# Performance work log

Measured on AMD Instinct MI355X. Metric: run time of the kernel, lower is better.

The kernel has to match this reference:

```python
import jax, jax.numpy as jnp
import numpy as np

N = 8192
D_IN = 512
D_HID = 256
D_OUT = 128
NEG_SLOPE = 0.25
MASK_VAL = -1.0e12
EDGE_PROB = 0.004  # avg degree ~33


def _leaky(x):
    return jax.nn.leaky_relu(x, NEG_SLOPE)


def setup_inputs() -> dict:
    key = jax.random.key(0)
    ks = jax.random.split(key, 9)
    x = jax.random.normal(ks[0], (N, D_IN), jnp.float32)
    # sparse-ish normalized adjacency, stored dense (torch uses sparse mm / to_dense)
    vals = jax.random.uniform(ks[1], (N, N), jnp.float32)
    mask = jax.random.uniform(ks[2], (N, N)) < EDGE_PROB
    adj = jnp.where(mask, vals, 0.0).astype(jnp.float32)
    W1 = jax.random.normal(ks[3], (D_IN, D_HID), jnp.float32) * (2.0 / (D_IN + D_HID)) ** 0.5
    b1 = jnp.zeros((D_HID,), jnp.float32)
    W2 = jax.random.normal(ks[4], (D_HID, D_HID), jnp.float32) * (1.0 / D_HID) ** 0.5
    b2 = jnp.zeros((D_HID,), jnp.float32)
    Wg = jax.random.normal(ks[5], (D_HID, D_OUT), jnp.float32) * (2.0 / (D_HID + D_OUT)) ** 0.5
    a = jax.random.normal(ks[6], (2 * D_OUT, 1), jnp.float32) * 0.1
    return dict(x=x, adj=adj, W1=W1, b1=b1, W2=W2, b2=b2, Wg=Wg, a=a)


def reference(x, adj, W1, b1, W2, b2, Wg, a):
    # GCN layer 1: adj @ (x @ W1) + b1, leaky_relu (dropout p=0 / eval -> identity)
    x1 = _leaky(adj @ (x @ W1) + b1)
    # GCN layer 2
    x2 = _leaky(adj @ (x1 @ W2) + b2)
    # GAT layer: h = x2 @ Wg; e[i,j] = leaky_relu([h_i || h_j] @ a)
    # identical to leaky_relu((h@a1)_i + (h@a2)_j) without the O(N^2*2F) concat
    h = x2 @ Wg                              # [N, D_OUT]
    a1 = a[:D_OUT, 0]
    a2 = a[D_OUT:, 0]
    e = _leaky((h @ a1)[:, None] + (h @ a2)[None, :])  # [N, N]
    att = jnp.where(adj > 0, e, MASK_VAL)
    att = jax.nn.softmax(att, axis=1)
    h_prime = att @ h                        # [N, D_OUT] (concat=False -> no elu)
    out = _leaky(h_prime)
    mu = out[:, : D_OUT // 2]
    logvar = out[:, D_OUT // 2 :]
    return mu, logvar
```

## Files before the change

kernel.cpp:

```cpp
#include <hip/hip_runtime.h>

typedef unsigned short u16;
typedef __bf16 bf16x8 __attribute__((ext_vector_type(8)));
typedef float f32x4 __attribute__((ext_vector_type(4)));

#define NROW 8192
#define CAP 128
#define D_IN 512
#define D_HID 256
#define D_OUT 128

__device__ __forceinline__ float leaky_f(float x) { return x > 0.f ? x : 0.25f * x; }

__device__ __forceinline__ u16 f2bf_rne(float f) {
  unsigned u = __float_as_uint(f);
  u += 0x7fffu + ((u >> 16) & 1u);
  return (u16)(u >> 16);
}
__device__ __forceinline__ void split_bf16(float f, u16& hi, u16& lo) {
  hi = f2bf_rne(f);
  float fh = __uint_as_float(((unsigned)hi) << 16);
  lo = f2bf_rne(f - fh);
}

__global__ __launch_bounds__(256) void k_csr(const float* __restrict__ adj,
    int* __restrict__ cnt, int* __restrict__ cols, float* __restrict__ vals) {
  int i = blockIdx.x;
  __shared__ int c;
  if (threadIdx.x == 0) c = 0;
  __syncthreads();
  const float4* row = (const float4*)(adj + (size_t)i * NROW);
  for (int j4 = threadIdx.x; j4 < NROW / 4; j4 += 256) {
    float4 v = row[j4];
    int base = j4 * 4;
    if (v.x > 0.f) { int s = atomicAdd(&c, 1); if (s < CAP) { cols[i*CAP+s] = base;   vals[i*CAP+s] = v.x; } }
    if (v.y > 0.f) { int s = atomicAdd(&c, 1); if (s < CAP) { cols[i*CAP+s] = base+1; vals[i*CAP+s] = v.y; } }
    if (v.z > 0.f) { int s = atomicAdd(&c, 1); if (s < CAP) { cols[i*CAP+s] = base+2; vals[i*CAP+s] = v.z; } }
    if (v.w > 0.f) { int s = atomicAdd(&c, 1); if (s < CAP) { cols[i*CAP+s] = base+3; vals[i*CAP+s] = v.w; } }
  }
  __syncthreads();
  if (threadIdx.x == 0) cnt[i] = (c < CAP) ? c : CAP;
}

__global__ __launch_bounds__(256) void k_pack_x(const float* __restrict__ X, u16* __restrict__ Ap) {
  size_t id = (size_t)blockIdx.x * 256 + threadIdx.x;
  int k = (int)(id & 511);
  size_t i = id >> 9;
  float f = X[id];
  u16 hi, lo; split_bf16(f, hi, lo);
  size_t ro = i * 1536;
  Ap[ro + k] = hi; Ap[ro + 512 + k] = hi; Ap[ro + 1024 + k] = lo;
}

__global__ __launch_bounds__(256) void k_pack_w(const float* __restrict__ W, u16* __restrict__ Bt,
                                                int K, int Nc) {
  int id = blockIdx.x * 256 + threadIdx.x;
  if (id >= K * Nc) return;
  int n = id % Nc, k = id / Nc;
  float f = W[id];
  u16 hi, lo; split_bf16(f, hi, lo);
  size_t ro = (size_t)n * 3 * K;
  Bt[ro + k] = hi; Bt[ro + K + k] = lo; Bt[ro + 2*K + k] = hi;
}

__global__ __launch_bounds__(256) void k_gemm(const u16* __restrict__ A, const u16* __restrict__ Bt,
    float* __restrict__ C, int N, int K) {
  __shared__ u16 As[64][40];
  __shared__ u16 Bs[64][40];
  int tid = threadIdx.x;
  int bm = blockIdx.y * 64, bn = blockIdx.x * 64;
  int wave = tid >> 6, lane = tid & 63, l15 = lane & 15, quad = lane >> 4;
  f32x4 acc[4] = {};
  int r = tid >> 2, kc = (tid & 3) << 3;
  for (int k0 = 0; k0 < K; k0 += 32) {
    uint4 av = *(const uint4*)(A + (size_t)(bm + r) * K + k0 + kc);
    uint4 bv = *(const uint4*)(Bt + (size_t)(bn + r) * K + k0 + kc);
    *(uint4*)(&As[r][kc]) = av;
    *(uint4*)(&Bs[r][kc]) = bv;
    __syncthreads();
    bf16x8 af = *(const bf16x8*)(&As[wave * 16 + l15][quad * 8]);
#pragma unroll
    for (int c2 = 0; c2 < 4; ++c2) {
      bf16x8 bfr = *(const bf16x8*)(&Bs[c2 * 16 + l15][quad * 8]);
      acc[c2] = __builtin_amdgcn_mfma_f32_16x16x32_bf16(af, bfr, acc[c2], 0, 0, 0);
    }
    __syncthreads();
  }
#pragma unroll
  for (int c2 = 0; c2 < 4; ++c2)
#pragma unroll
    for (int rg = 0; rg < 4; ++rg) {
      int rowi = bm + wave * 16 + quad * 4 + rg;
      int coli = bn + c2 * 16 + l15;
      C[(size_t)rowi * N + coli] = acc[c2][rg];
    }
}

__global__ __launch_bounds__(256) void k_spmm_pack(const float* __restrict__ Hin,
    const float* __restrict__ bias, const int* __restrict__ cnt,
    const int* __restrict__ cols, const float* __restrict__ vals, u16* __restrict__ Ap) {
  int i = blockIdx.x, t = threadIdx.x;
  __shared__ int sc[CAP];
  __shared__ float sv[CAP];
  int n = cnt[i];
  if (t < n) { sc[t] = cols[i * CAP + t]; sv[t] = vals[i * CAP + t]; }
  __syncthreads();
  float acc = bias[t];
  for (int k = 0; k < n; ++k)
    acc = fmaf(sv[k], Hin[(size_t)sc[k] * D_HID + t], acc);
  acc = leaky_f(acc);
  u16 hi, lo; split_bf16(acc, hi, lo);
  size_t ro = (size_t)i * 768;
  Ap[ro + t] = hi; Ap[ro + 256 + t] = hi; Ap[ro + 512 + t] = lo;
}

__global__ __launch_bounds__(64) void k_sdot(const float* __restrict__ h,
    const float* __restrict__ a, float* __restrict__ s1, float* __restrict__ s2) {
  int i = blockIdx.x, t = threadIdx.x;
  float v0 = h[(size_t)i * D_OUT + t], v1 = h[(size_t)i * D_OUT + 64 + t];
  float p1 = v0 * a[t] + v1 * a[64 + t];
  float p2 = v0 * a[128 + t] + v1 * a[192 + t];
  for (int o = 32; o > 0; o >>= 1) { p1 += __shfl_down(p1, o); p2 += __shfl_down(p2, o); }
  if (t == 0) { s1[i] = p1; s2[i] = p2; }
}

__global__ __launch_bounds__(128) void k_attn(const float* __restrict__ h,
    const float* __restrict__ s1, const float* __restrict__ s2,
    const int* __restrict__ cnt, const int* __restrict__ cols, float* __restrict__ out) {
  int i = blockIdx.x, t = threadIdx.x;
  __shared__ int sc[CAP];
  __shared__ float sw[CAP];
  __shared__ float sred[2];
  int n = cnt[i];
  float s1i = s1[i];
  if (t < n) { int c = cols[i * CAP + t]; sc[t] = c; sw[t] = leaky_f(s1i + s2[c]); }
  __syncthreads();
  if (t < 64) {
    float m = -1e30f;
    if (t < n) m = sw[t];
    if (t + 64 < n) m = fmaxf(m, sw[t + 64]);
    for (int o = 32; o > 0; o >>= 1) m = fmaxf(m, __shfl_down(m, o));
    if (t == 0) sred[0] = m;
  }
  __syncthreads();
  float mx = sred[0];
  if (t < n) sw[t] = expf(sw[t] - mx);
  __syncthreads();
  if (t < 64) {
    float s = 0.f;
    if (t < n) s = sw[t];
    if (t + 64 < n) s += sw[t + 64];
    for (int o = 32; o > 0; o >>= 1) s += __shfl_down(s, o);
    if (t == 0) sred[1] = s;
  }
  __syncthreads();
  float inv = (n > 0) ? 1.0f / sred[1] : 0.f;
  float acc = 0.f;
  for (int k = 0; k < n; ++k)
    acc = fmaf(sw[k], h[(size_t)sc[k] * D_OUT + t], acc);
  acc = leaky_f(acc * inv);
  if (t < 64) out[(size_t)i * 64 + t] = acc;
  else        out[(size_t)NROW * 64 + (size_t)i * 64 + (t - 64)] = acc;
}

extern "C" void kernel_launch(void* const* d_in, const int* in_sizes, int n_in,
                              void* d_out, int out_size, void* d_ws, size_t ws_size,
                              hipStream_t stream) {
  const float* x   = (const float*)d_in[0];
  const float* adj = (const float*)d_in[1];
  const float* W1  = (const float*)d_in[2];
  const float* b1  = (const float*)d_in[3];
  const float* W2  = (const float*)d_in[4];
  const float* b2  = (const float*)d_in[5];
  const float* Wg  = (const float*)d_in[6];
  const float* a   = (const float*)d_in[7];
  float* out = (float*)d_out;

  char* ws = (char*)d_ws;
  int*   row_cnt  = (int*)  (ws + 0);
  int*   row_cols = (int*)  (ws + 32768);
  float* row_vals = (float*)(ws + 4227072);
  u16*   B1t      = (u16*)  (ws + 8421376);
  u16*   B2t      = (u16*)  (ws + 9207808);
  u16*   B3t      = (u16*)  (ws + 9601024);
  float* s1       = (float*)(ws + 9797632);
  float* s2       = (float*)(ws + 9830400);
  float* h        = (float*)(ws + 9863168);
  float* H0T2     = (float*)(ws + 14057472);
  u16*   Apack    = (u16*)  (ws + 22446080);

  k_csr<<<NROW, 256, 0, stream>>>(adj, row_cnt, row_cols, row_vals);
  k_pack_x<<<(NROW * D_IN) / 256, 256, 0, stream>>>(x, Apack);
  k_pack_w<<<(D_IN * D_HID + 255) / 256, 256, 0, stream>>>(W1, B1t, D_IN, D_HID);
  k_pack_w<<<(D_HID * D_HID + 255) / 256, 256, 0, stream>>>(W2, B2t, D_HID, D_HID);
  k_pack_w<<<(D_HID * D_OUT + 255) / 256, 256, 0, stream>>>(Wg, B3t, D_HID, D_OUT);
  k_gemm<<<dim3(D_HID / 64, NROW / 64), 256, 0, stream>>>(Apack, B1t, H0T2, D_HID, 3 * D_IN);
  k_spmm_pack<<<NROW, 256, 0, stream>>>(H0T2, b1, row_cnt, row_cols, row_vals, Apack);
  k_gemm<<<dim3(D_HID / 64, NROW / 64), 256, 0, stream>>>(Apack, B2t, H0T2, D_HID, 3 * D_HID);
  k_spmm_pack<<<NROW, 256, 0, stream>>>(H0T2, b2, row_cnt, row_cols, row_vals, Apack);
  k_gemm<<<dim3(D_OUT / 64, NROW / 64), 256, 0, stream>>>(Apack, B3t, h, D_OUT, 3 * D_HID);
  k_sdot<<<NROW, 64, 0, stream>>>(h, a, s1, s2);
  k_attn<<<NROW, 128, 0, stream>>>(h, s1, s2, row_cnt, row_cols, out);
}
```

Baseline: 527.5 us.

## Enlarge GEMM tiles to 128x64 with K-step 64 and merge pack kernels

The split-bf16 GEMM now computes a 128x64 output tile per block, with each wave holding a 2x4 grid of MFMA accumulators. The K step grows from 32 to 64 and the LDS rows are padded to 72 elements, so each synchronisation covers more MFMA work and each B fragment is reused across two A fragments. The four packing kernels are merged into one launch that branches on block index. The tradeoff is higher register use, which may lower occupancy, and half as many blocks in the grid.

Result: no change. 517.9 us (-1.8%).

```diff
diff --git a/kernel.cpp b/kernel.cpp
--- a/kernel.cpp
+++ b/kernel.cpp
@@ -42,19 +42,25 @@
   if (threadIdx.x == 0) cnt[i] = (c < CAP) ? c : CAP;
 }
 
-__global__ __launch_bounds__(256) void k_pack_x(const float* __restrict__ X, u16* __restrict__ Ap) {
-  size_t id = (size_t)blockIdx.x * 256 + threadIdx.x;
-  int k = (int)(id & 511);
-  size_t i = id >> 9;
-  float f = X[id];
-  u16 hi, lo; split_bf16(f, hi, lo);
-  size_t ro = i * 1536;
-  Ap[ro + k] = hi; Ap[ro + 512 + k] = hi; Ap[ro + 1024 + k] = lo;
-}
-
-__global__ __launch_bounds__(256) void k_pack_w(const float* __restrict__ W, u16* __restrict__ Bt,
-                                                int K, int Nc) {
-  int id = blockIdx.x * 256 + threadIdx.x;
+__global__ __launch_bounds__(256) void k_pack_all(const float* __restrict__ X, u16* __restrict__ Ap,
+    const float* __restrict__ W1, u16* __restrict__ B1,
+    const float* __restrict__ W2, u16* __restrict__ B2,
+    const float* __restrict__ Wg, u16* __restrict__ B3) {
+  int b = blockIdx.x;
+  if (b < 16384) {
+    size_t id = (size_t)b * 256 + threadIdx.x;
+    int k = (int)(id & 511);
+    size_t i = id >> 9;
+    float f = X[id];
+    u16 hi, lo; split_bf16(f, hi, lo);
+    size_t ro = i * 1536;
+    Ap[ro + k] = hi; Ap[ro + 512 + k] = hi; Ap[ro + 1024 + k] = lo;
+    return;
+  }
+  const float* W; u16* Bt; int K, Nc, id;
+  if (b < 16896)      { W = W1; Bt = B1; K = D_IN;  Nc = D_HID; id = (b - 16384) * 256 + threadIdx.x; }
+  else if (b < 17152) { W = W2; Bt = B2; K = D_HID; Nc = D_HID; id = (b - 16896) * 256 + threadIdx.x; }
+  else                { W = Wg; Bt = B3; K = D_HID; Nc = D_OUT; id = (b - 17152) * 256 + threadIdx.x; }
   if (id >= K * Nc) return;
   int n = id % Nc, k = id / Nc;
   float f = W[id];
@@ -65,35 +71,51 @@
 
 __global__ __launch_bounds__(256) void k_gemm(const u16* __restrict__ A, const u16* __restrict__ Bt,
     float* __restrict__ C, int N, int K) {
-  __shared__ u16 As[64][40];
-  __shared__ u16 Bs[64][40];
+  __shared__ u16 As[128 * 72];
+  __shared__ u16 Bs[64 * 72];
   int tid = threadIdx.x;
-  int bm = blockIdx.y * 64, bn = blockIdx.x * 64;
+  int bm = blockIdx.y * 128, bn = blockIdx.x * 64;
   int wave = tid >> 6, lane = tid & 63, l15 = lane & 15, quad = lane >> 4;
-  f32x4 acc[4] = {};
-  int r = tid >> 2, kc = (tid & 3) << 3;
-  for (int k0 = 0; k0 < K; k0 += 32) {
-    uint4 av = *(const uint4*)(A + (size_t)(bm + r) * K + k0 + kc);
-    uint4 bv = *(const uint4*)(Bt + (size_t)(bn + r) * K + k0 + kc);
-    *(uint4*)(&As[r][kc]) = av;
-    *(uint4*)(&Bs[r][kc]) = bv;
+  f32x4 acc[2][4] = {};
+  int ar = tid >> 1, ac = (tid & 1) * 32;
+  int br = tid >> 2, bc = (tid & 3) * 16;
+  const u16* Arow = A + (size_t)(bm + ar) * K + ac;
+  const u16* Brow = Bt + (size_t)(bn + br) * K + bc;
+  for (int k0 = 0; k0 < K; k0 += 64) {
+#pragma unroll
+    for (int j = 0; j < 4; ++j)
+      *(uint4*)(&As[ar * 72 + ac + j * 8]) = *(const uint4*)(Arow + k0 + j * 8);
+#pragma unroll
+    for (int j = 0; j < 2; ++j)
+      *(uint4*)(&Bs[br * 72 + bc + j * 8]) = *(const uint4*)(Brow + k0 + j * 8);
     __syncthreads();
-    bf16x8 af = *(const bf16x8*)(&As[wave * 16 + l15][quad * 8]);
-#pragma unroll
-    for (int c2 = 0; c2 < 4; ++c2) {
-      bf16x8 bfr = *(const bf16x8*)(&Bs[c2 * 16 + l15][quad * 8]);
-      acc[c2] = __builtin_amdgcn_mfma_f32_16x16x32_bf16(af, bfr, acc[c2], 0, 0, 0);
+#pragma unroll
+    for (int kk = 0; kk < 64; kk += 32) {
+      bf16x8 af[2], bf[4];
+#pragma unroll
+      for (int r = 0; r < 2; ++r)
+        af[r] = *(const bf16x8*)(&As[(wave * 32 + r * 16 + l15) * 72 + kk + quad * 8]);
+#pragma unroll
+      for (int c = 0; c < 4; ++c)
+        bf[c] = *(const bf16x8*)(&Bs[(c * 16 + l15) * 72 + kk + quad * 8]);
+#pragma unroll
+      for (int r = 0; r < 2; ++r)
+#pragma unroll
+        for (int c = 0; c < 4; ++c)
+          acc[r][c] = __builtin_amdgcn_mfma_f32_16x16x32_bf16(af[r], bf[c], acc[r][c], 0, 0, 0);
     }
     __syncthreads();
   }
 #pragma unroll
-  for (int c2 = 0; c2 < 4; ++c2)
-#pragma unroll
-    for (int rg = 0; rg < 4; ++rg) {
-      int rowi = bm + wave * 16 + quad * 4 + rg;
-      int coli = bn + c2 * 16 + l15;
-      C[(size_t)rowi * N + coli] = acc[c2][rg];
-    }
+  for (int r = 0; r < 2; ++r)
+#pragma unroll
+    for (int c = 0; c < 4; ++c)
+#pragma unroll
+      for (int rg = 0; rg < 4; ++rg) {
+        int rowi = bm + wave * 32 + r * 16 + quad * 4 + rg;
+        int coli = bn + c * 16 + l15;
+        C[(size_t)rowi * N + coli] = acc[r][c][rg];
+      }
 }
 
 __global__ __launch_bounds__(256) void k_spmm_pack(const float* __restrict__ Hin,
@@ -190,15 +212,12 @@
   u16*   Apack    = (u16*)  (ws + 22446080);
 
   k_csr<<<NROW, 256, 0, stream>>>(adj, row_cnt, row_cols, row_vals);
-  k_pack_x<<<(NROW * D_IN) / 256, 256, 0, stream>>>(x, Apack);
-  k_pack_w<<<(D_IN * D_HID + 255) / 256, 256, 0, stream>>>(W1, B1t, D_IN, D_HID);
-  k_pack_w<<<(D_HID * D_HID + 255) / 256, 256, 0, stream>>>(W2, B2t, D_HID, D_HID);
-  k_pack_w<<<(D_HID * D_OUT + 255) / 256, 256, 0, stream>>>(Wg, B3t, D_HID, D_OUT);
-  k_gemm<<<dim3(D_HID / 64, NROW / 64), 256, 0, stream>>>(Apack, B1t, H0T2, D_HID, 3 * D_IN);
+  k_pack_all<<<17280, 256, 0, stream>>>(x, Apack, W1, B1t, W2, B2t, Wg, B3t);
+  k_gemm<<<dim3(D_HID / 64, NROW / 128), 256, 0, stream>>>(Apack, B1t, H0T2, D_HID, 3 * D_IN);
   k_spmm_pack<<<NROW, 256, 0, stream>>>(H0T2, b1, row_cnt, row_cols, row_vals, Apack);
-  k_gemm<<<dim3(D_HID / 64, NROW / 64), 256, 0, stream>>>(Apack, B2t, H0T2, D_HID, 3 * D_HID);
+  k_gemm<<<dim3(D_HID / 64, NROW / 128), 256, 0, stream>>>(Apack, B2t, H0T2, D_HID, 3 * D_HID);
   k_spmm_pack<<<NROW, 256, 0, stream>>>(H0T2, b2, row_cnt, row_cols, row_vals, Apack);
-  k_gemm<<<dim3(D_OUT / 64, NROW / 64), 256, 0, stream>>>(Apack, B3t, h, D_OUT, 3 * D_HID);
+  k_gemm<<<dim3(D_OUT / 64, NROW / 128), 256, 0, stream>>>(Apack, B3t, h, D_OUT, 3 * D_HID);
   k_sdot<<<NROW, 64, 0, stream>>>(h, a, s1, s2);
   k_attn<<<NROW, 128, 0, stream>>>(h, s1, s2, row_cnt, row_cols, out);
 }
```
